# Kernel tuning notes

Hardware: AMD Instinct MI355X
Metric: run time of the kernel (lower is better)

The kernel has to match this reference:

```python
import jax, jax.numpy as jnp
import numpy as np

GRID_SIZE = 5
SPLINE_ORDER = 3
IN_SIZE = 257
HID = 40
NUM_LAYERS = 2
OUT_SIZE = 257
N_BASIS = GRID_SIZE + SPLINE_ORDER  # 8


def make_grid():
    # efficient-kan extended grid over [-1, 1]
    h = 2.0 / GRID_SIZE
    return (jnp.arange(-SPLINE_ORDER, GRID_SIZE + SPLINE_ORDER + 1, dtype=jnp.float32) * h - 1.0)


def b_splines(x, grid):
    # x: (..., in), grid: (G + 2k + 1,) -> (..., in, G + k) via Cox-de Boor
    x = x[..., None]
    b = ((x >= grid[:-1]) & (x < grid[1:])).astype(x.dtype)
    for k in range(1, SPLINE_ORDER + 1):
        b = ((x - grid[: -(k + 1)]) / (grid[k:-1] - grid[: -(k + 1)]) * b[..., :-1]
             + (grid[k + 1:] - x) / (grid[k + 1:] - grid[1:-k]) * b[..., 1:])
    return b


def gru_cell(x, h, Wih, Whh, bih, bhh):
    # torch.nn.GRUCell math, applied to every timestep at once.
    # x: (B,T,I), h: (B,T,H); Wih: (3H,I), Whh: (3H,H)
    gi = jnp.einsum('bti,gi->btg', x, Wih) + bih
    gh = jnp.einsum('bth,gh->btg', h, Whh) + bhh
    i_r, i_z, i_n = jnp.split(gi, 3, axis=-1)
    h_r, h_z, h_n = jnp.split(gh, 3, axis=-1)
    r = jax.nn.sigmoid(i_r + h_r)
    z = jax.nn.sigmoid(i_z + h_z)
    n = jnp.tanh(i_n + r * h_n)
    return (1.0 - z) * n + z * h


def kan_linear(x, base_weight, spline_weight, spline_scaler, grid):
    # efficient-kan KANLinear: SiLU base branch + B-spline branch
    base = jnp.einsum('bti,oi->bto', jax.nn.silu(x), base_weight)
    basis = b_splines(x, grid)  # (B,T,in,N_BASIS)
    w = spline_weight * spline_scaler[..., None]  # (out,in,N_BASIS)
    spl = jnp.einsum('btim,oim->bto', basis, w)
    return base + spl


def setup_inputs() -> dict:
    key = jax.random.key(0)
    ks = jax.random.split(key, 16)
    B, T = 64, 1000
    s = 0.1
    inp = {
        'x': jax.random.normal(ks[0], (B, T, IN_SIZE), dtype=jnp.float32),
        'Wih_f': jax.random.normal(ks[1], (NUM_LAYERS, 3 * HID, IN_SIZE), dtype=jnp.float32) * s,
        'Whh_f': jax.random.normal(ks[2], (NUM_LAYERS, 3 * HID, HID), dtype=jnp.float32) * s,
        'bih_f': jax.random.normal(ks[3], (NUM_LAYERS, 3 * HID), dtype=jnp.float32) * s,
        'bhh_f': jax.random.normal(ks[4], (NUM_LAYERS, 3 * HID), dtype=jnp.float32) * s,
        'Wih_b': jax.random.normal(ks[5], (NUM_LAYERS, 3 * HID, IN_SIZE), dtype=jnp.float32) * s,
        'Whh_b': jax.random.normal(ks[6], (NUM_LAYERS, 3 * HID, HID), dtype=jnp.float32) * s,
        'bih_b': jax.random.normal(ks[7], (NUM_LAYERS, 3 * HID), dtype=jnp.float32) * s,
        'bhh_b': jax.random.normal(ks[8], (NUM_LAYERS, 3 * HID), dtype=jnp.float32) * s,
        'base_weight': jax.random.normal(ks[9], (OUT_SIZE, 2 * HID), dtype=jnp.float32) * s,
        'spline_weight': jax.random.normal(ks[10], (OUT_SIZE, 2 * HID, N_BASIS), dtype=jnp.float32) * s,
        'spline_scaler': jnp.ones((OUT_SIZE, 2 * HID), dtype=jnp.float32),
        'slope': jnp.ones((OUT_SIZE,), dtype=jnp.float32),
        'lengths': jnp.full((B,), T, dtype=jnp.int32),
    }
    return inp


def reference(x, Wih_f, Whh_f, bih_f, bhh_f, Wih_b, Whh_b, bih_b, bhh_b,
              base_weight, spline_weight, spline_scaler, slope, lengths):
    B, T, _ = x.shape
    grid = make_grid()
    zeros_h = jnp.zeros((B, T, HID), dtype=x.dtype)
    # Forward-direction stack: layer 1 sees zero hidden (ht_f[0] is never
    # written in the source), layer 2 sees layer 1's same-timestep output.
    hf = zeros_h
    for l in range(NUM_LAYERS):
        hf = gru_cell(x, hf, Wih_f[l], Whh_f[l], bih_f[l], bhh_f[l])
    # Backward direction consumes x in reversed time order; out[:, i] pairs
    # hf(time i) with hb computed from x[:, T-1-i], i.e. hb in loop order.
    xb = x[:, ::-1, :]
    hb = zeros_h
    for l in range(NUM_LAYERS):
        hb = gru_cell(xb, hb, Wih_b[l], Whh_b[l], bih_b[l], bhh_b[l])
    feat = jnp.concatenate([hf, hb], axis=-1)  # (B,T,2H) == ht[-1]
    out = kan_linear(feat, base_weight, spline_weight, spline_scaler, grid)
    out = 1.2 * jax.nn.sigmoid(slope * out)
    return out
```

## Files before the change

### kernel.cpp

```cpp
#include <hip/hip_runtime.h>
#include <hip/hip_bf16.h>

#define B_    64
#define T_    1000
#define IN_   257
#define HID_  40
#define G3_   120
#define OUT_  257
#define M_    (B_*T_)
#define NGI_  480
#define KP_   736
#define KP1_  288
#define NP_   288

#define OFF_GI1 30720000ull
#define OFF_P   61440000ull
#define OFF_WK  (OFF_P + 94208000ull)
#define OFF_WB  (OFF_WK + 423936ull)
#define OFF_WHT (OFF_WB + 276480ull)
#define OFF_H0R (OFF_WHT + 32768ull)
#define OFF_H0C (OFF_H0R + 16384000ull)
#define OFF_GHC (OFF_H0C + 10240000ull)

typedef __attribute__((ext_vector_type(8))) short bfx8;
typedef __attribute__((ext_vector_type(4))) short bfx4;
typedef __attribute__((ext_vector_type(4))) float f32x4;

__device__ __forceinline__ float sigf(float x){ return 1.0f/(1.0f + __expf(-x)); }
__device__ __forceinline__ float tanhfast(float x){ return 1.0f - 2.0f/(__expf(2.0f*x)+1.0f); }

__device__ __forceinline__ short bfbits(float v){
    __hip_bfloat16 h = __float2bfloat16(v);
    return *(short*)&h;
}
__device__ __forceinline__ float b2f(short s){
    return __uint_as_float(((unsigned)(unsigned short)s) << 16);
}

__global__ __launch_bounds__(256) void kprep(const float* __restrict__ bw,
                                             const float* __restrict__ sw,
                                             const float* __restrict__ ss,
                                             __hip_bfloat16* __restrict__ wk){
    int idx = blockIdx.x*256 + threadIdx.x;
    if (idx >= NP_*(KP_/8)) return;
    int o = idx / (KP_/8), q = idx % (KP_/8);
    bfx8 pk;
#pragma unroll
    for (int e=0;e<8;e++){
        int k = q*8 + e;
        float v = 0.0f;
        if (o < OUT_ && k < 720){
            if (k < 80) v = bw[o*80 + k];
            else { int i = (k-80)>>3, m = (k-80)&7; v = sw[(o*80+i)*8 + m] * ss[o*80+i]; }
        }
        pk[e] = bfbits(v);
    }
    *(bfx8*)((void*)&wk[(size_t)o*KP_ + q*8]) = pk;
}

__global__ __launch_bounds__(256) void wprep(const float* __restrict__ Wf,
                                             const float* __restrict__ Wbk,
                                             const float* __restrict__ Whh_f,
                                             const float* __restrict__ Whh_b,
                                             const float* __restrict__ bhh_f,
                                             const float* __restrict__ bhh_b,
                                             __hip_bfloat16* __restrict__ wb,
                                             __hip_bfloat16* __restrict__ wht){
    int idx = blockIdx.x*256 + threadIdx.x;
    if (idx < NGI_*(KP1_/8)){
        int n = idx / (KP1_/8), q = idx % (KP1_/8);
        bfx8 pk;
#pragma unroll
        for (int e=0;e<8;e++){
            int k = q*8 + e;
            float v = 0.0f;
            if (k < IN_) v = (n < 240) ? Wf[(size_t)n*IN_ + k] : Wbk[(size_t)(n-240)*IN_ + k];
            pk[e] = bfbits(v);
        }
        *(bfx8*)((void*)&wb[(size_t)n*KP1_ + q*8]) = pk;
        return;
    }
    int i2 = idx - NGI_*(KP1_/8);
    if (i2 >= 2*128*8) return;
    int d = i2 >> 10;
    int rest = i2 & 1023;
    int gate = rest >> 3, q = rest & 7;
    const float* Whh = d ? Whh_b : Whh_f;
    const float* bhh = d ? bhh_b : bhh_f;
    bfx8 pk;
#pragma unroll
    for (int e=0;e<8;e++){
        int k = q*8 + e;
        float v = 0.0f;
        if (gate < G3_){
            if (k < 40) v = Whh[G3_*HID_ + gate*HID_ + k];
            else if (k == 40) v = bhh[G3_ + gate];
        }
        pk[e] = bfbits(v);
    }
    *(bfx8*)((void*)&wht[(size_t)(d*128 + gate)*64 + q*8]) = pk;
}

__global__ __launch_bounds__(512) void k1_gemm(const float* __restrict__ X,
                                               const __hip_bfloat16* __restrict__ Wb16,
                                               const float* __restrict__ bf,
                                               const float* __restrict__ bb,
                                               __hip_bfloat16* __restrict__ gi0,
                                               __hip_bfloat16* __restrict__ gi1){
    __shared__ __hip_bfloat16 Asm[2][256*40];
    __shared__ __hip_bfloat16 Bsm[2][160*40];
    int tid = threadIdx.x, wave = tid>>6, lane = tid&63;
    int wr = wave>>1, wc = wave&1;
    int rl = lane&15, kq = lane>>4;
    int m0 = blockIdx.y*256, n0 = blockIdx.x*160;

    int rA = tid>>2, qA = tid&3;
    f32x4 acc[4][5];
#pragma unroll
    for (int f=0;f<4;f++)
#pragma unroll
        for (int j=0;j<5;j++) acc[f][j] = (f32x4){0.f,0.f,0.f,0.f};

    bfx8 ra[2], rb[2];

#define K1_LOAD(tt) { \
    int k0 = (tt)*32; \
    _Pragma("unroll") \
    for (int p=0;p<2;p++){ \
        int r = rA + p*128; \
        int kg = k0 + qA*8; \
        const float* xp = &X[(size_t)(m0+r)*IN_ + kg]; \
        if (kg + 7 < IN_){ \
            f32x4 x0 = *(const f32x4*)xp; \
            f32x4 x1 = *(const f32x4*)(xp+4); \
            _Pragma("unroll") \
            for (int e=0;e<4;e++){ ra[p][e] = bfbits(x0[e]); ra[p][4+e] = bfbits(x1[e]); } \
        } else { \
            _Pragma("unroll") \
            for (int e=0;e<8;e++){ int k = kg + e; ra[p][e] = (k < IN_) ? bfbits(xp[e]) : (short)0; } \
        } \
    } \
    rb[0] = *(const bfx8*)&Wb16[(size_t)(n0+rA)*KP1_ + k0 + qA*8]; \
    if (tid < 128) rb[1] = *(const bfx8*)&Wb16[(size_t)(n0+128+rA)*KP1_ + k0 + qA*8]; }

#define K1_WRITE(bufi) { \
    *(bfx8*)((void*)&Asm[bufi][rA*40 + qA*8]) = ra[0]; \
    *(bfx8*)((void*)&Asm[bufi][(rA+128)*40 + qA*8]) = ra[1]; \
    *(bfx8*)((void*)&Bsm[bufi][rA*40 + qA*8]) = rb[0]; \
    if (tid < 128) *(bfx8*)((void*)&Bsm[bufi][(rA+128)*40 + qA*8]) = rb[1]; }

    K1_LOAD(0); K1_WRITE(0); __syncthreads();
    for (int t=0; t<9; ++t){
        int c = t&1;
        if (t < 8) K1_LOAD(t+1);
        bfx8 a[4];
#pragma unroll
        for (int f=0;f<4;f++)
            a[f] = *(bfx8*)((void*)&Asm[c][(wr*64 + f*16 + rl)*40 + kq*8]);
#pragma unroll
        for (int j=0;j<5;j++){
            bfx8 b = *(bfx8*)((void*)&Bsm[c][(wc*80 + j*16 + rl)*40 + kq*8]);
#pragma unroll
            for (int f=0;f<4;f++)
                acc[f][j] = __builtin_amdgcn_mfma_f32_16x16x32_bf16(a[f], b, acc[f][j], 0,0,0);
        }
        if (t < 8) K1_WRITE(c^1);
        __syncthreads();
    }
#pragma unroll
    for (int j=0;j<5;j++){
        int n = n0 + wc*80 + j*16 + rl;
        float bias = (n < 240) ? bf[n] : bb[n-240];
        int d  = (n >= 240) ? 1 : 0;
        int nn = n - 240*d;
#pragma unroll
        for (int f=0;f<4;f++){
            int mb = m0 + wr*64 + f*16 + kq*4;
            bfx4 v;
#pragma unroll
            for (int r=0;r<4;r++) v[r] = bfbits(acc[f][j][r] + bias);
            if (nn < 120){
                *(bfx4*)((void*)&gi0[(size_t)(d*120 + nn)*M_ + mb]) = v;
            } else {
                *(bfx4*)((void*)&gi1[(size_t)(d*120 + nn - 120)*M_ + mb]) = v;
            }
        }
    }
}

__global__ __launch_bounds__(256) void k2a(const __hip_bfloat16* __restrict__ gi0,
                                           const float* __restrict__ bhh_f,
                                           const float* __restrict__ bhh_b,
                                           __hip_bfloat16* __restrict__ h0R,
                                           __hip_bfloat16* __restrict__ h0C){
    int blk = blockIdx.x;
    int dir = (blk >= 250) ? 1 : 0;
    int m = (blk - dir*250)*256 + threadIdx.x;
    int b = m / T_, t = m - b*T_;
    int src = dir ? (b*T_ + (T_-1-t)) : m;
    const float* bhh0v = dir ? bhh_b : bhh_f;

    const __hip_bfloat16* g0 = gi0 + (size_t)(dir*120)*M_ + src;
    __hip_bfloat16* hc = h0C + (size_t)(dir*40)*M_ + m;
    float h0[HID_];
#pragma unroll
    for (int j=0;j<HID_;j++){
        float ir = b2f(*(const short*)&g0[(size_t)j*M_]);
        float iz = b2f(*(const short*)&g0[(size_t)(40+j)*M_]);
        float in = b2f(*(const short*)&g0[(size_t)(80+j)*M_]);
        float r = sigf(ir + bhh0v[j]);
        float z = sigf(iz + bhh0v[40+j]);
        float n = tanhfast(in + r*bhh0v[80+j]);
        h0[j] = (1.0f - z)*n;
        hc[(size_t)j*M_] = __float2bfloat16(h0[j]);
    }
    __hip_bfloat16* hr = h0R + (size_t)(dir*M_ + m)*64;
#pragma unroll
    for (int q=0;q<8;q++){
        bfx8 v;
#pragma unroll
        for (int e=0;e<8;e++){
            int idx = q*8 + e;
            float f = (idx < HID_) ? h0[idx] : (idx == HID_ ? 1.0f : 0.0f);
            v[e] = bfbits(f);
        }
        *(bfx8*)((void*)&hr[q*8]) = v;
    }
}

__global__ __launch_bounds__(512) void k2b(const __hip_bfloat16* __restrict__ h0R,
                                           const __hip_bfloat16* __restrict__ WhT,
                                           __hip_bfloat16* __restrict__ ghC){
    __shared__ __hip_bfloat16 Ah[256*64];
    __shared__ __hip_bfloat16 Bh[128*64];
    int tid = threadIdx.x, wave = tid>>6, lane = tid&63;
    int wr = wave>>1, wc = wave&1;
    int rl = lane&15, kq = lane>>4;
    int blk = blockIdx.x;
    int dir = (blk >= 250) ? 1 : 0;
    int m0 = (blk - dir*250)*256;

#pragma unroll
    for (int p=0;p<4;p++){
        int c = tid + p*512;
        int row = c>>3, q = c&7;
        bfx8 v = *(const bfx8*)&h0R[(size_t)(dir*M_ + m0 + row)*64 + q*8];
        *(bfx8*)((void*)&Ah[row*64 + ((q ^ (row&7))<<3)]) = v;
    }
#pragma unroll
    for (int p=0;p<2;p++){
        int c = tid + p*512;
        int row = c>>3, q = c&7;
        bfx8 v = *(const bfx8*)&WhT[(size_t)(dir*128 + row)*64 + q*8];
        *(bfx8*)((void*)&Bh[row*64 + ((q ^ (row&7))<<3)]) = v;
    }
    __syncthreads();

    f32x4 acc[4][4];
#pragma unroll
    for (int f=0;f<4;f++)
#pragma unroll
        for (int j=0;j<4;j++) acc[f][j] = (f32x4){0.f,0.f,0.f,0.f};

#pragma unroll
    for (int ks=0;ks<2;ks++){
        bfx8 a[4], bb[4];
#pragma unroll
        for (int f=0;f<4;f++){
            int row = wr*64 + f*16 + rl;
            a[f] = *(bfx8*)((void*)&Ah[row*64 + (((ks*4+kq) ^ (row&7))<<3)]);
        }
#pragma unroll
        for (int j=0;j<4;j++){
            int row = wc*64 + j*16 + rl;
            bb[j] = *(bfx8*)((void*)&Bh[row*64 + (((ks*4+kq) ^ (row&7))<<3)]);
        }
#pragma unroll
        for (int f=0;f<4;f++)
#pragma unroll
            for (int j=0;j<4;j++)
                acc[f][j] = __builtin_amdgcn_mfma_f32_16x16x32_bf16(a[f], bb[j], acc[f][j], 0,0,0);
    }
#pragma unroll
    for (int j=0;j<4;j++){
        int n = wc*64 + j*16 + rl;
        if (n < G3_){
#pragma unroll
            for (int f=0;f<4;f++){
                int mb = m0 + wr*64 + f*16 + kq*4;
                bfx4 v;
#pragma unroll
                for (int r=0;r<4;r++) v[r] = bfbits(acc[f][j][r]);
                *(bfx4*)((void*)&ghC[(size_t)(dir*G3_ + n)*M_ + mb]) = v;
            }
        }
    }
}

__global__ __launch_bounds__(256, 4) void k2c(const __hip_bfloat16* __restrict__ gi1,
                                              const __hip_bfloat16* __restrict__ ghC,
                                              const __hip_bfloat16* __restrict__ h0C,
                                              __hip_bfloat16* __restrict__ P){
    int tid = threadIdx.x;
    int bb = blockIdx.x;
    int mblk = bb % 250;
    int rest = bb / 250;
    int dir = rest / 5, grp = rest % 5;
    int m = mblk*256 + tid;
    int b = m / T_, t = m - b*T_;
    int src = dir ? (b*T_ + (T_-1-t)) : m;

    const __hip_bfloat16* g1 = gi1 + (size_t)(dir*120)*M_ + src;
    const __hip_bfloat16* gh = ghC + (size_t)(dir*120)*M_ + m;
    const __hip_bfloat16* hc = h0C + (size_t)(dir*40)*M_ + m;

    bfx8 sil;
#pragma unroll
    for (int jj=0;jj<8;jj++){
        int j = grp*8 + jj;
        float ir = b2f(*(const short*)&g1[(size_t)j*M_]);
        float iz = b2f(*(const short*)&g1[(size_t)(40+j)*M_]);
        float in = b2f(*(const short*)&g1[(size_t)(80+j)*M_]);
        float gr = b2f(*(const short*)&gh[(size_t)j*M_]);
        float gz = b2f(*(const short*)&gh[(size_t)(40+j)*M_]);
        float gn = b2f(*(const short*)&gh[(size_t)(80+j)*M_]);
        float r = sigf(ir + gr);
        float z = sigf(iz + gz);
        float n = tanhfast(in + r*gn);
        float h1 = (1.0f - z)*n + z*b2f(*(const short*)&hc[(size_t)j*M_]);
        sil[jj] = bfbits(h1 * sigf(h1));

        float tt = (h1 + 1.0f) * 2.5f;
        float fs = floorf(tt);
        fs = fminf(fmaxf(fs, 0.0f), 4.0f);
        int sp = (int)fs;
        float u  = tt - fs;
        float um = 1.0f - u;
        float u2 = u*u, u3 = u2*u;
        float N0 = um*um*um * (1.0f/6.0f);
        float N1 = (3.0f*u3 - 6.0f*u2 + 4.0f) * (1.0f/6.0f);
        float N2 = (-3.0f*u3 + 3.0f*u2 + 3.0f*u + 1.0f) * (1.0f/6.0f);
        float N3 = u3 * (1.0f/6.0f);
        bfx8 pk;
#pragma unroll
        for (int i=0;i<8;i++){
            int d = i - sp;
            float v = (d==0)?N0 : (d==1)?N1 : (d==2)?N2 : (d==3)?N3 : 0.0f;
            pk[i] = bfbits(v);
        }
        *(bfx8*)((void*)&P[((size_t)(10 + dir*40 + j)*M_ + m)*8]) = pk;
    }
    *(bfx8*)((void*)&P[((size_t)(dir*5 + grp)*M_ + m)*8]) = sil;
    if (dir==0 && grp==0){
        bfx8 z8 = {0,0,0,0,0,0,0,0};
        *(bfx8*)((void*)&P[((size_t)90*M_ + m)*8]) = z8;
        *(bfx8*)((void*)&P[((size_t)91*M_ + m)*8]) = z8;
    }
}

__global__ __launch_bounds__(512) void k3_gemm(const __hip_bfloat16* __restrict__ P,
                                               const __hip_bfloat16* __restrict__ Wk,
                                               const float* __restrict__ slope,
                                               float* __restrict__ outp){
    __shared__ __hip_bfloat16 Asm[2][256*40];
    __shared__ __hip_bfloat16 Bsm[2][NP_*40];
    int tid = threadIdx.x, wave = tid>>6, lane = tid&63;
    int wr = wave>>1, wc = wave&1;
    int rl = lane&15, kq = lane>>4;
    int m0 = blockIdx.x*256;

    int qA = tid>>8, rA = tid&255;
    int rB = tid>>2, qB = tid&3;

    f32x4 acc[4][9];
#pragma unroll
    for (int f=0;f<4;f++)
#pragma unroll
        for (int j=0;j<9;j++) acc[f][j] = (f32x4){0.f,0.f,0.f,0.f};

    bfx8 ra[2], rb[3];

#define K3_LOAD(tt) { \
    int k8 = (tt)*4, k0 = (tt)*32; \
    ra[0] = *(const bfx8*)&P[((size_t)(k8+qA)*M_ + m0 + rA)*8]; \
    ra[1] = *(const bfx8*)&P[((size_t)(k8+qA+2)*M_ + m0 + rA)*8]; \
    rb[0] = *(const bfx8*)&Wk[(size_t)rB*KP_ + k0 + qB*8]; \
    rb[1] = *(const bfx8*)&Wk[(size_t)(rB+128)*KP_ + k0 + qB*8]; \
    if (tid < 128) rb[2] = *(const bfx8*)&Wk[(size_t)(rB+256)*KP_ + k0 + qB*8]; }

#define K3_WRITE(bufi) { \
    *(bfx8*)((void*)&Asm[bufi][rA*40 + qA*8]) = ra[0]; \
    *(bfx8*)((void*)&Asm[bufi][rA*40 + (qA+2)*8]) = ra[1]; \
    *(bfx8*)((void*)&Bsm[bufi][rB*40 + qB*8]) = rb[0]; \
    *(bfx8*)((void*)&Bsm[bufi][(rB+128)*40 + qB*8]) = rb[1]; \
    if (tid < 128) *(bfx8*)((void*)&Bsm[bufi][(rB+256)*40 + qB*8]) = rb[2]; }

    K3_LOAD(0); K3_WRITE(0); __syncthreads();
    for (int t=0; t<23; ++t){
        int c = t&1;
        if (t < 22) K3_LOAD(t+1);
        bfx8 a[4];
#pragma unroll
        for (int f=0;f<4;f++)
            a[f] = *(bfx8*)((void*)&Asm[c][(wr*64 + f*16 + rl)*40 + kq*8]);
#pragma unroll
        for (int j=0;j<9;j++){
            bfx8 b = *(bfx8*)((void*)&Bsm[c][(wc*144 + j*16 + rl)*40 + kq*8]);
#pragma unroll
            for (int f=0;f<4;f++)
                acc[f][j] = __builtin_amdgcn_mfma_f32_16x16x32_bf16(a[f], b, acc[f][j], 0,0,0);
        }
        if (t < 22) K3_WRITE(c^1);
        __syncthreads();
    }
#pragma unroll
    for (int j=0;j<9;j++){
        int n = wc*144 + j*16 + rl;
        if (n < OUT_){
            float sl = slope[n];
#pragma unroll
            for (int f=0;f<4;f++){
                int mb = m0 + wr*64 + f*16 + kq*4;
#pragma unroll
                for (int r=0;r<4;r++)
                    outp[(size_t)(mb+r)*OUT_ + n] = 1.2f * sigf(sl*acc[f][j][r]);
            }
        }
    }
}

extern "C" void kernel_launch(void* const* d_in, const int* in_sizes, int n_in,
                              void* d_out, int out_size, void* d_ws, size_t ws_size,
                              hipStream_t stream) {
    const float* x      = (const float*)d_in[0];
    const float* Wih_f  = (const float*)d_in[1];
    const float* Whh_f  = (const float*)d_in[2];
    const float* bih_f  = (const float*)d_in[3];
    const float* bhh_f  = (const float*)d_in[4];
    const float* Wih_b  = (const float*)d_in[5];
    const float* Whh_b  = (const float*)d_in[6];
    const float* bih_b  = (const float*)d_in[7];
    const float* bhh_b  = (const float*)d_in[8];
    const float* base_w = (const float*)d_in[9];
    const float* spl_w  = (const float*)d_in[10];
    const float* spl_s  = (const float*)d_in[11];
    const float* slope  = (const float*)d_in[12];

    char* ws = (char*)d_ws;
    __hip_bfloat16* gi0 = (__hip_bfloat16*)ws;
    __hip_bfloat16* gi1 = (__hip_bfloat16*)(ws + OFF_GI1);
    __hip_bfloat16* P   = (__hip_bfloat16*)(ws + OFF_P);
    __hip_bfloat16* Wk  = (__hip_bfloat16*)(ws + OFF_WK);
    __hip_bfloat16* Wb  = (__hip_bfloat16*)(ws + OFF_WB);
    __hip_bfloat16* WhT = (__hip_bfloat16*)(ws + OFF_WHT);
    __hip_bfloat16* h0R = (__hip_bfloat16*)(ws + OFF_H0R);
    __hip_bfloat16* h0C = (__hip_bfloat16*)(ws + OFF_H0C);
    __hip_bfloat16* ghC = (__hip_bfloat16*)(ws + OFF_GHC);
    float* outp = (float*)d_out;

    hipLaunchKernelGGL(kprep, dim3((NP_*(KP_/8) + 255)/256), dim3(256), 0, stream,
                       base_w, spl_w, spl_s, Wk);
    hipLaunchKernelGGL(wprep, dim3((NGI_*(KP1_/8) + 2048 + 255)/256), dim3(256), 0, stream,
                       Wih_f, Wih_b, Whh_f, Whh_b, bhh_f, bhh_b, Wb, WhT);
    hipLaunchKernelGGL(k1_gemm, dim3(3, 250), dim3(512), 0, stream,
                       x, Wb, bih_f, bih_b, gi0, gi1);
    hipLaunchKernelGGL(k2a, dim3(500), dim3(256), 0, stream,
                       gi0, bhh_f, bhh_b, h0R, h0C);
    hipLaunchKernelGGL(k2b, dim3(500), dim3(512), 0, stream,
                       h0R, WhT, ghC);
    hipLaunchKernelGGL(k2c, dim3(2500), dim3(256), 0, stream,
                       gi1, ghC, h0C, P);
    hipLaunchKernelGGL(k3_gemm, dim3(250), dim3(512), 0, stream,
                       P, Wk, slope, outp);
}
```

Measured before the change: 326.9 us.

## Restructure input GEMM to load X once per block and stream weights from global

The input-projection GEMM now gives each 256-thread block 64 rows and all 480 output columns. The block's whole K extent of X is converted to bf16 and staged in shared memory once. B fragments are read directly from global memory (L2-resident weights) instead of being double-buffered through LDS. This removes the three-fold re-reading and re-conversion of X across column blocks and the per-k-step barriers. In exchange each wave now holds 30 accumulators, which raises register pressure, and the weights are fetched from global memory with no LDS reuse.

```diff
diff --git a/kernel.cpp b/kernel.cpp
--- a/kernel.cpp
+++ b/kernel.cpp
@@ -101,81 +101,66 @@
     *(bfx8*)((void*)&wht[(size_t)(d*128 + gate)*64 + q*8]) = pk;
 }
 
-__global__ __launch_bounds__(512) void k1_gemm(const float* __restrict__ X,
+__global__ __launch_bounds__(256) void k1_gemm(const float* __restrict__ X,
                                                const __hip_bfloat16* __restrict__ Wb16,
                                                const float* __restrict__ bf,
                                                const float* __restrict__ bb,
                                                __hip_bfloat16* __restrict__ gi0,
                                                __hip_bfloat16* __restrict__ gi1){
-    __shared__ __hip_bfloat16 Asm[2][256*40];
-    __shared__ __hip_bfloat16 Bsm[2][160*40];
+    __shared__ __hip_bfloat16 Asm[9*64*40];
     int tid = threadIdx.x, wave = tid>>6, lane = tid&63;
     int wr = wave>>1, wc = wave&1;
     int rl = lane&15, kq = lane>>4;
-    int m0 = blockIdx.y*256, n0 = blockIdx.x*160;
-
-    int rA = tid>>2, qA = tid&3;
-    f32x4 acc[4][5];
-#pragma unroll
-    for (int f=0;f<4;f++)
-#pragma unroll
-        for (int j=0;j<5;j++) acc[f][j] = (f32x4){0.f,0.f,0.f,0.f};
-
-    bfx8 ra[2], rb[2];
-
-#define K1_LOAD(tt) { \
-    int k0 = (tt)*32; \
-    _Pragma("unroll") \
-    for (int p=0;p<2;p++){ \
-        int r = rA + p*128; \
-        int kg = k0 + qA*8; \
-        const float* xp = &X[(size_t)(m0+r)*IN_ + kg]; \
-        if (kg + 7 < IN_){ \
-            f32x4 x0 = *(const f32x4*)xp; \
-            f32x4 x1 = *(const f32x4*)(xp+4); \
-            _Pragma("unroll") \
-            for (int e=0;e<4;e++){ ra[p][e] = bfbits(x0[e]); ra[p][4+e] = bfbits(x1[e]); } \
-        } else { \
-            _Pragma("unroll") \
-            for (int e=0;e<8;e++){ int k = kg + e; ra[p][e] = (k < IN_) ? bfbits(xp[e]) : (short)0; } \
-        } \
-    } \
-    rb[0] = *(const bfx8*)&Wb16[(size_t)(n0+rA)*KP1_ + k0 + qA*8]; \
-    if (tid < 128) rb[1] = *(const bfx8*)&Wb16[(size_t)(n0+128+rA)*KP1_ + k0 + qA*8]; }
-
-#define K1_WRITE(bufi) { \
-    *(bfx8*)((void*)&Asm[bufi][rA*40 + qA*8]) = ra[0]; \
-    *(bfx8*)((void*)&Asm[bufi][(rA+128)*40 + qA*8]) = ra[1]; \
-    *(bfx8*)((void*)&Bsm[bufi][rA*40 + qA*8]) = rb[0]; \
-    if (tid < 128) *(bfx8*)((void*)&Bsm[bufi][(rA+128)*40 + qA*8]) = rb[1]; }
-
-    K1_LOAD(0); K1_WRITE(0); __syncthreads();
-    for (int t=0; t<9; ++t){
-        int c = t&1;
-        if (t < 8) K1_LOAD(t+1);
-        bfx8 a[4];
-#pragma unroll
-        for (int f=0;f<4;f++)
-            a[f] = *(bfx8*)((void*)&Asm[c][(wr*64 + f*16 + rl)*40 + kq*8]);
-#pragma unroll
-        for (int j=0;j<5;j++){
-            bfx8 b = *(bfx8*)((void*)&Bsm[c][(wc*80 + j*16 + rl)*40 + kq*8]);
-#pragma unroll
-            for (int f=0;f<4;f++)
-                acc[f][j] = __builtin_amdgcn_mfma_f32_16x16x32_bf16(a[f], b, acc[f][j], 0,0,0);
-        }
-        if (t < 8) K1_WRITE(c^1);
-        __syncthreads();
-    }
-#pragma unroll
-    for (int j=0;j<5;j++){
-        int n = n0 + wc*80 + j*16 + rl;
+    int m0 = blockIdx.x*64;
+
+    {
+        int r = tid>>2, slot = tid&3;
+#pragma unroll
+        for (int ks=0;ks<9;ks++){
+            int kg = ks*32 + slot*8;
+            const float* xp = &X[(size_t)(m0+r)*IN_ + kg];
+            bfx8 pk;
+            if (kg + 7 < IN_){
+                f32x4 x0 = *(const f32x4*)xp;
+                f32x4 x1 = *(const f32x4*)(xp+4);
+#pragma unroll
+                for (int e=0;e<4;e++){ pk[e] = bfbits(x0[e]); pk[4+e] = bfbits(x1[e]); }
+            } else {
+#pragma unroll
+                for (int e=0;e<8;e++){ int k = kg + e; pk[e] = (k < IN_) ? bfbits(xp[e]) : (short)0; }
+            }
+            *(bfx8*)((void*)&Asm[(ks*64 + r)*40 + slot*8]) = pk;
+        }
+    }
+    __syncthreads();
+
+    f32x4 acc[2][15];
+#pragma unroll
+    for (int f=0;f<2;f++)
+#pragma unroll
+        for (int j=0;j<15;j++) acc[f][j] = (f32x4){0.f,0.f,0.f,0.f};
+
+    for (int ks=0; ks<9; ++ks){
+        bfx8 a0 = *(bfx8*)((void*)&Asm[(ks*64 + wr*32 + rl)*40 + kq*8]);
+        bfx8 a1 = *(bfx8*)((void*)&Asm[(ks*64 + wr*32 + 16 + rl)*40 + kq*8]);
+        const __hip_bfloat16* bp = &Wb16[(size_t)(wc*240 + rl)*KP1_ + ks*32 + kq*8];
+#pragma unroll
+        for (int j=0;j<15;j++){
+            bfx8 b = *(const bfx8*)&bp[(size_t)j*16*KP1_];
+            acc[0][j] = __builtin_amdgcn_mfma_f32_16x16x32_bf16(a0, b, acc[0][j], 0,0,0);
+            acc[1][j] = __builtin_amdgcn_mfma_f32_16x16x32_bf16(a1, b, acc[1][j], 0,0,0);
+        }
+    }
+
+#pragma unroll
+    for (int j=0;j<15;j++){
+        int n = wc*240 + j*16 + rl;
         float bias = (n < 240) ? bf[n] : bb[n-240];
         int d  = (n >= 240) ? 1 : 0;
         int nn = n - 240*d;
 #pragma unroll
-        for (int f=0;f<4;f++){
-            int mb = m0 + wr*64 + f*16 + kq*4;
+        for (int f=0;f<2;f++){
+            int mb = m0 + wr*32 + f*16 + kq*4;
             bfx4 v;
 #pragma unroll
             for (int r=0;r<4;r++) v[r] = bfbits(acc[f][j][r] + bias);
@@ -462,7 +447,7 @@
                        base_w, spl_w, spl_s, Wk);
     hipLaunchKernelGGL(wprep, dim3((NGI_*(KP1_/8) + 2048 + 255)/256), dim3(256), 0, stream,
                        Wih_f, Wih_b, Whh_f, Whh_b, bhh_f, bhh_b, Wb, WhT);
-    hipLaunchKernelGGL(k1_gemm, dim3(3, 250), dim3(512), 0, stream,
+    hipLaunchKernelGGL(k1_gemm, dim3(1000), dim3(256), 0, stream,
                        x, Wb, bih_f, bih_b, gi0, gi1);
     hipLaunchKernelGGL(k2a, dim3(500), dim3(256), 0, stream,
                        gi0, bhh_f, bhh_b, h0R, h0C);
```

Measured after the change: 364.8 us. 11.6% more time.
